# Kernel tuning notes

Measured on AMD Instinct MI355X. Metric: run time of the kernel, lower is better.

## Reference

```python
import jax, jax.numpy as jnp
import numpy as np
from jax import lax

B, T, I, H = 64, 1024, 128, 512
DT = 0.1
EPS = 1e-8
BIG_CLAMP = 50.0
W_SCALE = 0.02  # small init so safe_exp gates stay well-behaved


def _safe_exp(v):
    return jnp.exp(jnp.minimum(v, BIG_CLAMP))


def setup_inputs() -> dict:
    key = jax.random.key(0)
    ks = jax.random.split(key, 9)
    w = lambda k, shape: jax.random.normal(k, shape, jnp.float32) * W_SCALE
    z = lambda: jnp.zeros((H,), jnp.float32)
    return {
        "x": jax.random.normal(ks[0], (B, T, I), jnp.float32),
        "Wsw": w(ks[1], (H, I)), "bsw": z(),
        "Wsm": w(ks[2], (H, I)), "bsm": z(),
        "Wss": w(ks[3], (H, I)), "bss": z(),
        "Wiw": w(ks[4], (H, H)), "biw": z(),
        "Wim": w(ks[5], (H, H)), "bim": z(),
        "Wis": w(ks[6], (H, H)), "bis": z(),
        "Wtcx": w(ks[7], (H, I)),  # time_constant weight, input slice
        "Wtch": w(ks[8], (H, H)),  # time_constant weight, hidden slice
        "btc": z(),
    }


def reference(x, Wsw, bsw, Wsm, bsm, Wss, bss,
              Wiw, biw, Wim, bim, Wis, bis, Wtcx, Wtch, btc):
    # Precompute all x-dependent projections as big GEMMs over (B,T).
    sw = jnp.einsum('bti,hi->bth', x, Wsw) + bsw
    smu = jnp.einsum('bti,hi->bth', x, Wsm) + bsm
    ssig = jnp.einsum('bti,hi->bth', x, Wss) + bss
    sensory = sw * jax.nn.sigmoid(smu) * _safe_exp(ssig)      # (B,T,H)
    tcx = jnp.einsum('bti,hi->bth', x, Wtcx) + btc            # (B,T,H)

    def step(h, inp):
        sens_t, tcx_t = inp                                   # each (B,H)
        tau = jax.nn.softplus(tcx_t + h @ Wtch.T) + 0.1
        inter = (h @ Wiw.T + biw) \
            * jax.nn.sigmoid(h @ Wim.T + bim) \
            * _safe_exp(h @ Wis.T + bis)
        dh_dt = (sens_t + inter - h) / jnp.maximum(tau, EPS)
        h_new = h + DT * dh_dt
        return h_new, h_new

    h0 = jnp.ones((B, H), x.dtype)
    xs = (jnp.swapaxes(sensory, 0, 1), jnp.swapaxes(tcx, 0, 1))  # (T,B,H)
    _, ys = lax.scan(step, h0, xs)
    return jnp.swapaxes(ys, 0, 1)  # (B,T,H)
```

## Files before the change

kernel.cpp:

```cpp
#include <hip/hip_runtime.h>
#include <math.h>

#define NB 64
#define NT 1024
#define NI 128
#define NH 512

typedef unsigned long long u64;

__global__ __launch_bounds__(256) void prep_kernel(
    const float* __restrict__ Wsw, const float* __restrict__ Wsm,
    const float* __restrict__ Wss, const float* __restrict__ Wtcx,
    float* __restrict__ WT_in, u64* __restrict__ htag)
{
  int idx = blockIdx.x * blockDim.x + threadIdx.x;
  int np  = gridDim.x * blockDim.x;
  for (int i = idx; i < NH * NI; i += np) {
    int j = i >> 7, k = i & 127;
    int o = k * 2048 + j * 4;
    WT_in[o + 0] = Wsw[i];
    WT_in[o + 1] = Wsm[i];
    WT_in[o + 2] = Wss[i];
    WT_in[o + 3] = Wtcx[i];
  }
  for (int i = idx; i < 2 * NB * NH; i += np) htag[i] = 0x3F800000ULL;
}

__global__ __launch_bounds__(256, 2) void phase1_kernel(
    const float* __restrict__ x, const float* __restrict__ WT_in,
    const float* __restrict__ bsw, const float* __restrict__ bsm,
    const float* __restrict__ bss, const float* __restrict__ btc,
    float* __restrict__ sens, float* __restrict__ tcx)
{
  __shared__ __align__(16) float xs[32 * NI];
  const int tid = threadIdx.x;
  const int n0  = blockIdx.x * 32;

  const float4* xsrc = (const float4*)(x + (size_t)n0 * NI);
#pragma unroll
  for (int i = 0; i < 4; i++)
    ((float4*)xs)[i * 256 + tid] = xsrc[i * 256 + tid];
  __syncthreads();

  for (int jj = 0; jj < 2; jj++) {
    const int j = tid + jj * 256;
    float4 acc[32];
#pragma unroll
    for (int n = 0; n < 32; n++) acc[n] = make_float4(0.f, 0.f, 0.f, 0.f);

    const float4* wp = (const float4*)WT_in + j;
#pragma unroll 2
    for (int k = 0; k < NI; k++) {
      float4 w = wp[(size_t)k * 512];
#pragma unroll
      for (int n = 0; n < 32; n++) {
        float xv = xs[n * NI + k];
        acc[n].x = fmaf(xv, w.x, acc[n].x);
        acc[n].y = fmaf(xv, w.y, acc[n].y);
        acc[n].z = fmaf(xv, w.z, acc[n].z);
        acc[n].w = fmaf(xv, w.w, acc[n].w);
      }
    }
    const float b0 = bsw[j], b1 = bsm[j], b2v = bss[j], b3 = btc[j];
#pragma unroll 4
    for (int n = 0; n < 32; n++) {
      float sw = acc[n].x + b0;
      float sm = acc[n].y + b1;
      float ss = acc[n].z + b2v;
      float tc = acc[n].w + b3;
      float sig = 1.f / (1.f + expf(-sm));
      float se  = expf(fminf(ss, 50.f));
      size_t o = (size_t)(n0 + n) * NH + j;
      sens[o] = sw * sig * se;
      tcx[o]  = tc;
    }
  }
}

__global__ __launch_bounds__(256, 1) void phase2_kernel(
    const float* __restrict__ Wiw, const float* __restrict__ Wim,
    const float* __restrict__ Wis, const float* __restrict__ Wtch,
    const float* __restrict__ biw, const float* __restrict__ bim,
    const float* __restrict__ bis,
    const float* __restrict__ tcx, float* __restrict__ out,
    u64* __restrict__ htag)
{
  __shared__ __align__(16) float hl[8 * 576];
  __shared__ float red[4 * 528];

  const int tid = threadIdx.x;
  const int wv  = tid >> 6;
  const int ln  = tid & 63;
  const int bg  = blockIdx.x & 7;
  const int js  = blockIdx.x >> 3;

  const int cg = ln & 15;
  const int r  = wv * 4 + (ln >> 4);
  const int k0 = r << 5;

  const int g   = cg & 3;
  const int jl0 = cg >> 2;
  const float* Wp = (g == 0) ? Wiw : (g == 1) ? Wim : (g == 2) ? Wis : Wtch;
  float wreg[4][32];
#pragma unroll
  for (int ci = 0; ci < 4; ci++) {
    const float* wrow = Wp + (size_t)(js * 16 + jl0 + 4 * ci) * NH + k0;
#pragma unroll
    for (int kk = 0; kk < 32; kk++) wreg[ci][kk] = wrow[kk];
  }

  const int ejl = tid & 15;
  const int eb  = tid >> 4;
  const int ej  = js * 16 + ejl;
  float bw = 0.f, bm = 0.f, bs = 0.f;
  if (tid < 128) { bw = biw[ej]; bm = bim[ej]; bs = bis[ej]; }

  u64* const hgrp0 = htag + bg * 4096;
  u64* const hgrp1 = htag + NB * NH + bg * 4096;

  for (int t = 0; t < NT; t++) {
    u64* hsrc = (t & 1) ? hgrp1 : hgrp0;
    u64* hdst = (t & 1) ? hgrp0 : hgrp1;
    const unsigned want = (unsigned)t;

    float sens_v = 0.f, tcx_v = 0.f;
    size_t eidx = 0;
    if (tid < 128) {
      eidx   = ((size_t)(bg * 8 + eb) * NT + t) * NH + ej;
      sens_v = out[eidx];
      tcx_v  = tcx[eidx];
    }

    u64 w[16];
#pragma unroll
    for (int i = 0; i < 16; i++)
      w[i] = __hip_atomic_load(hsrc + i * 256 + tid, __ATOMIC_RELAXED,
                               __HIP_MEMORY_SCOPE_AGENT);
    for (;;) {
      bool ok = true;
#pragma unroll
      for (int i = 0; i < 16; i++) ok = ok && ((unsigned)(w[i] >> 32) == want);
      if (ok) break;
      __builtin_amdgcn_s_sleep(2);
#pragma unroll
      for (int i = 0; i < 16; i++)
        if ((unsigned)(w[i] >> 32) != want)
          w[i] = __hip_atomic_load(hsrc + i * 256 + tid, __ATOMIC_RELAXED,
                                   __HIP_MEMORY_SCOPE_AGENT);
    }

#pragma unroll
    for (int i = 0; i < 16; i++) {
      int f  = i * 256 + tid;
      int b2 = f >> 9, k = f & 511;
      hl[b2 * 576 + (k >> 5) * 36 + (k & 31)] =
          __uint_as_float((unsigned)(w[i] & 0xFFFFFFFFull));
    }
    __syncthreads();

    float acc[4][8];
#pragma unroll
    for (int ci = 0; ci < 4; ci++)
#pragma unroll
      for (int b2 = 0; b2 < 8; b2++) acc[ci][b2] = 0.f;

    const float* hb = hl + r * 36;
#pragma unroll
    for (int b2 = 0; b2 < 8; b2++) {
#pragma unroll
      for (int kc = 0; kc < 32; kc += 4) {
        float4 hv = *(const float4*)(hb + b2 * 576 + kc);
#pragma unroll
        for (int ci = 0; ci < 4; ci++) {
          acc[ci][b2] = fmaf(wreg[ci][kc + 0], hv.x, acc[ci][b2]);
          acc[ci][b2] = fmaf(wreg[ci][kc + 1], hv.y, acc[ci][b2]);
          acc[ci][b2] = fmaf(wreg[ci][kc + 2], hv.z, acc[ci][b2]);
          acc[ci][b2] = fmaf(wreg[ci][kc + 3], hv.w, acc[ci][b2]);
        }
      }
    }

#pragma unroll
    for (int ci = 0; ci < 4; ci++)
#pragma unroll
      for (int b2 = 0; b2 < 8; b2++) {
        float v = acc[ci][b2];
        v += __shfl_xor(v, 16, 64);
        v += __shfl_xor(v, 32, 64);
        acc[ci][b2] = v;
      }
    if (ln < 16) {
#pragma unroll
      for (int ci = 0; ci < 4; ci++)
#pragma unroll
        for (int b2 = 0; b2 < 8; b2++)
          red[wv * 528 + ln * 33 + ci * 8 + b2] = acc[ci][b2];
    }
    float h_old = 0.f;
    if (tid < 128) h_old = hl[eb * 576 + (ej >> 5) * 36 + (ej & 31)];
    __syncthreads();

    if (tid < 128) {
      float vals[4];
#pragma unroll
      for (int g2 = 0; g2 < 4; g2++) {
        int c = ejl * 4 + g2;
        int o = (c & 15) * 33 + (c >> 4) * 8 + eb;
        vals[g2] = red[o] + red[528 + o] + red[1056 + o] + red[1584 + o];
      }
      float iwv = vals[0] + bw;
      float imv = vals[1] + bm;
      float isv = vals[2] + bs;
      float tch = vals[3];
      float z   = tcx_v + tch;
      float tau = fmaxf(z, 0.f) + log1pf(expf(-fabsf(z))) + 0.1f;
      float sig = 1.f / (1.f + expf(-imv));
      float inter = iwv * sig * expf(fminf(isv, 50.f));
      float dh  = (sens_v + inter - h_old) / fmaxf(tau, 1e-8f);
      float hnew = h_old + 0.1f * dh;
      out[eidx] = hnew;
      u64 nw = ((u64)(unsigned)(t + 1) << 32) | (u64)__float_as_uint(hnew);
      __hip_atomic_store(hdst + eb * 512 + ej, nw, __ATOMIC_RELAXED,
                         __HIP_MEMORY_SCOPE_AGENT);
    }
  }
}

extern "C" void kernel_launch(void* const* d_in, const int* in_sizes, int n_in,
                              void* d_out, int out_size, void* d_ws, size_t ws_size,
                              hipStream_t stream) {
  const float* x    = (const float*)d_in[0];
  const float* Wsw  = (const float*)d_in[1];
  const float* bsw  = (const float*)d_in[2];
  const float* Wsm  = (const float*)d_in[3];
  const float* bsm  = (const float*)d_in[4];
  const float* Wss  = (const float*)d_in[5];
  const float* bss  = (const float*)d_in[6];
  const float* Wiw  = (const float*)d_in[7];
  const float* biw  = (const float*)d_in[8];
  const float* Wim  = (const float*)d_in[9];
  const float* bim  = (const float*)d_in[10];
  const float* Wis  = (const float*)d_in[11];
  const float* bis  = (const float*)d_in[12];
  const float* Wtcx = (const float*)d_in[13];
  const float* Wtch = (const float*)d_in[14];
  const float* btc  = (const float*)d_in[15];
  float* out = (float*)d_out;

  float* ws     = (float*)d_ws;
  float* WT_in  = ws;
  float* tcx    = ws + 262144;
  u64*   htag   = (u64*)(tcx + (size_t)NB * NT * NH);

  hipLaunchKernelGGL(prep_kernel, dim3(256), dim3(256), 0, stream,
                     Wsw, Wsm, Wss, Wtcx, WT_in, htag);

  hipLaunchKernelGGL(phase1_kernel, dim3(NB * NT / 32), dim3(256), 0, stream,
                     x, WT_in, bsw, bsm, bss, btc, out, tcx);

  hipLaunchKernelGGL(phase2_kernel, dim3(256), dim3(256), 0, stream,
                     Wiw, Wim, Wis, Wtch, biw, bim, bis,
                     tcx, out, htag);
}
```

Before: 8.124 ms.

## Replace tagged hidden-state polling with plain floats and a per-group arrival counter

Each recurrent step used to pack the step tag into the upper half of every 64-bit hidden-state word, and every thread spun on all 16 of its tagged words. Now the hidden state is stored as plain 32-bit floats. Each block drains its stores, then bumps one atomic counter per batch group, and readers spin only on that counter before bulk-loading the data. This halves the bytes exchanged per step and cuts polling traffic to a single address. In exchange it adds a block-wide barrier, a memory wait and an extra atomic round trip on the critical path of every step.

```diff
diff --git a/kernel.cpp b/kernel.cpp
--- a/kernel.cpp
+++ b/kernel.cpp
@@ -11,7 +11,8 @@
 __global__ __launch_bounds__(256) void prep_kernel(
     const float* __restrict__ Wsw, const float* __restrict__ Wsm,
     const float* __restrict__ Wss, const float* __restrict__ Wtcx,
-    float* __restrict__ WT_in, u64* __restrict__ htag)
+    float* __restrict__ WT_in, float* __restrict__ hdat,
+    unsigned* __restrict__ cnt)
 {
   int idx = blockIdx.x * blockDim.x + threadIdx.x;
   int np  = gridDim.x * blockDim.x;
@@ -23,7 +24,8 @@
     WT_in[o + 2] = Wss[i];
     WT_in[o + 3] = Wtcx[i];
   }
-  for (int i = idx; i < 2 * NB * NH; i += np) htag[i] = 0x3F800000ULL;
+  for (int i = idx; i < 2 * NB * NH; i += np) hdat[i] = 1.0f;
+  for (int i = idx; i < 256; i += np) cnt[i] = 0u;
 }
 
 __global__ __launch_bounds__(256, 2) void phase1_kernel(
@@ -83,7 +85,7 @@
     const float* __restrict__ biw, const float* __restrict__ bim,
     const float* __restrict__ bis,
     const float* __restrict__ tcx, float* __restrict__ out,
-    u64* __restrict__ htag)
+    float* __restrict__ hdat, unsigned* __restrict__ cnt)
 {
   __shared__ __align__(16) float hl[8 * 576];
   __shared__ float red[4 * 528];
@@ -115,13 +117,14 @@
   float bw = 0.f, bm = 0.f, bs = 0.f;
   if (tid < 128) { bw = biw[ej]; bm = bim[ej]; bs = bis[ej]; }
 
-  u64* const hgrp0 = htag + bg * 4096;
-  u64* const hgrp1 = htag + NB * NH + bg * 4096;
+  float* const hp0 = hdat + bg * 4096;
+  float* const hp1 = hdat + NB * NH + bg * 4096;
+  unsigned* const cbg = cnt + bg * 32;
 
   for (int t = 0; t < NT; t++) {
-    u64* hsrc = (t & 1) ? hgrp1 : hgrp0;
-    u64* hdst = (t & 1) ? hgrp0 : hgrp1;
-    const unsigned want = (unsigned)t;
+    const u64* dsrc = (const u64*)((t & 1) ? hp1 : hp0);
+    unsigned*  ddst = (unsigned*)((t & 1) ? hp0 : hp1);
+    const unsigned want = 32u * (unsigned)t;
 
     float sens_v = 0.f, tcx_v = 0.f;
     size_t eidx = 0;
@@ -131,30 +134,28 @@
       tcx_v  = tcx[eidx];
     }
 
-    u64 w[16];
-#pragma unroll
-    for (int i = 0; i < 16; i++)
-      w[i] = __hip_atomic_load(hsrc + i * 256 + tid, __ATOMIC_RELAXED,
+    if (t > 0) {
+      unsigned c;
+      do {
+        c = __hip_atomic_load(cbg, __ATOMIC_RELAXED, __HIP_MEMORY_SCOPE_AGENT);
+      } while (c < want);
+      asm volatile("" ::: "memory");
+    }
+
+    u64 w[8];
+#pragma unroll
+    for (int i = 0; i < 8; i++)
+      w[i] = __hip_atomic_load(dsrc + i * 256 + tid, __ATOMIC_RELAXED,
                                __HIP_MEMORY_SCOPE_AGENT);
-    for (;;) {
-      bool ok = true;
-#pragma unroll
-      for (int i = 0; i < 16; i++) ok = ok && ((unsigned)(w[i] >> 32) == want);
-      if (ok) break;
-      __builtin_amdgcn_s_sleep(2);
-#pragma unroll
-      for (int i = 0; i < 16; i++)
-        if ((unsigned)(w[i] >> 32) != want)
-          w[i] = __hip_atomic_load(hsrc + i * 256 + tid, __ATOMIC_RELAXED,
-                                   __HIP_MEMORY_SCOPE_AGENT);
-    }
-
-#pragma unroll
-    for (int i = 0; i < 16; i++) {
+
+#pragma unroll
+    for (int i = 0; i < 8; i++) {
       int f  = i * 256 + tid;
-      int b2 = f >> 9, k = f & 511;
-      hl[b2 * 576 + (k >> 5) * 36 + (k & 31)] =
-          __uint_as_float((unsigned)(w[i] & 0xFFFFFFFFull));
+      int b2 = f >> 8;
+      int k  = (f & 255) << 1;
+      float lo = __uint_as_float((unsigned)(w[i] & 0xFFFFFFFFull));
+      float hi = __uint_as_float((unsigned)(w[i] >> 32));
+      *(float2*)&hl[b2 * 576 + (k >> 5) * 36 + (k & 31)] = make_float2(lo, hi);
     }
     __syncthreads();
 
@@ -218,11 +219,15 @@
       float inter = iwv * sig * expf(fminf(isv, 50.f));
       float dh  = (sens_v + inter - h_old) / fmaxf(tau, 1e-8f);
       float hnew = h_old + 0.1f * dh;
+      __hip_atomic_store(ddst + eb * 512 + ej, __float_as_uint(hnew),
+                         __ATOMIC_RELAXED, __HIP_MEMORY_SCOPE_AGENT);
       out[eidx] = hnew;
-      u64 nw = ((u64)(unsigned)(t + 1) << 32) | (u64)__float_as_uint(hnew);
-      __hip_atomic_store(hdst + eb * 512 + ej, nw, __ATOMIC_RELAXED,
-                         __HIP_MEMORY_SCOPE_AGENT);
-    }
+      asm volatile("s_waitcnt vmcnt(0)" ::: "memory");
+    }
+    __syncthreads();
+    if (tid == 0)
+      __hip_atomic_fetch_add(cbg, 1u, __ATOMIC_RELAXED,
+                             __HIP_MEMORY_SCOPE_AGENT);
   }
 }
 
@@ -250,15 +255,16 @@
   float* ws     = (float*)d_ws;
   float* WT_in  = ws;
   float* tcx    = ws + 262144;
-  u64*   htag   = (u64*)(tcx + (size_t)NB * NT * NH);
+  float* hdat   = tcx + (size_t)NB * NT * NH;
+  unsigned* cnt = (unsigned*)(hdat + 2 * NB * NH);
 
   hipLaunchKernelGGL(prep_kernel, dim3(256), dim3(256), 0, stream,
-                     Wsw, Wsm, Wss, Wtcx, WT_in, htag);
+                     Wsw, Wsm, Wss, Wtcx, WT_in, hdat, cnt);
 
   hipLaunchKernelGGL(phase1_kernel, dim3(NB * NT / 32), dim3(256), 0, stream,
                      x, WT_in, bsw, bsm, bss, btc, out, tcx);
 
   hipLaunchKernelGGL(phase2_kernel, dim3(256), dim3(256), 0, stream,
                      Wiw, Wim, Wis, Wtch, biw, bim, bis,
-                     tcx, out, htag);
-}
+                     tcx, out, hdat, cnt);
+}
```

Result: faster. 7.535 ms (-7.2%).

## Interleave two batch groups per block to hide recurrent h-exchange latency

Applied to the files above, without the earlier changes.

The persistent recurrent kernel now runs 128 blocks, each owning two batch groups (bgA and bgB) with separate shared h buffers. While one group's step is being computed, the atomic loads that poll the other group's h tags are already in flight. Each block also issues the next step's loads for group A before finishing group B. The aim is to overlap the cross-block synchronisation latency with computation, at the cost of halving the block count so each block does twice the work per step. The poll sleep is shortened, and the output store now follows the tag publish.

```diff
diff --git a/kernel.cpp b/kernel.cpp
--- a/kernel.cpp
+++ b/kernel.cpp
@@ -77,6 +77,101 @@
   }
 }
 
+#define ISSUE16(W, SRC)                                                     \
+  _Pragma("unroll")                                                         \
+  for (int i = 0; i < 16; i++)                                              \
+    W[i] = __hip_atomic_load((SRC) + i * 256 + tid, __ATOMIC_RELAXED,       \
+                             __HIP_MEMORY_SCOPE_AGENT);
+
+#define CHECK16(W, SRC, WANT)                                               \
+  for (;;) {                                                                \
+    bool ok = true;                                                         \
+    _Pragma("unroll")                                                       \
+    for (int i = 0; i < 16; i++)                                            \
+      ok = ok && ((unsigned)(W[i] >> 32) == (WANT));                        \
+    if (ok) break;                                                          \
+    __builtin_amdgcn_s_sleep(1);                                            \
+    _Pragma("unroll")                                                       \
+    for (int i = 0; i < 16; i++)                                            \
+      if ((unsigned)(W[i] >> 32) != (WANT))                                 \
+        W[i] = __hip_atomic_load((SRC) + i * 256 + tid, __ATOMIC_RELAXED,   \
+                                 __HIP_MEMORY_SCOPE_AGENT);                 \
+  }
+
+#define DO_PHASE(HL, W, DST, EIDX, SENSV, TCXV, TP1)                        \
+  {                                                                         \
+    _Pragma("unroll")                                                       \
+    for (int i = 0; i < 16; i++) {                                          \
+      int f = i * 256 + tid;                                                \
+      int b2 = f >> 9, k = f & 511;                                         \
+      HL[b2 * 576 + (k >> 5) * 36 + (k & 31)] =                             \
+          __uint_as_float((unsigned)(W[i] & 0xFFFFFFFFull));                \
+    }                                                                       \
+    __syncthreads();                                                        \
+    float acc[4][8];                                                        \
+    _Pragma("unroll")                                                       \
+    for (int ci = 0; ci < 4; ci++)                                          \
+      _Pragma("unroll")                                                     \
+      for (int b2 = 0; b2 < 8; b2++) acc[ci][b2] = 0.f;                     \
+    const float* hb = HL + r * 36;                                          \
+    _Pragma("unroll")                                                       \
+    for (int b2 = 0; b2 < 8; b2++) {                                        \
+      _Pragma("unroll")                                                     \
+      for (int kc = 0; kc < 32; kc += 4) {                                  \
+        float4 hv = *(const float4*)(hb + b2 * 576 + kc);                   \
+        _Pragma("unroll")                                                   \
+        for (int ci = 0; ci < 4; ci++) {                                    \
+          acc[ci][b2] = fmaf(wreg[ci][kc + 0], hv.x, acc[ci][b2]);          \
+          acc[ci][b2] = fmaf(wreg[ci][kc + 1], hv.y, acc[ci][b2]);          \
+          acc[ci][b2] = fmaf(wreg[ci][kc + 2], hv.z, acc[ci][b2]);          \
+          acc[ci][b2] = fmaf(wreg[ci][kc + 3], hv.w, acc[ci][b2]);          \
+        }                                                                   \
+      }                                                                     \
+    }                                                                       \
+    _Pragma("unroll")                                                       \
+    for (int ci = 0; ci < 4; ci++)                                          \
+      _Pragma("unroll")                                                     \
+      for (int b2 = 0; b2 < 8; b2++) {                                      \
+        float v = acc[ci][b2];                                              \
+        v += __shfl_xor(v, 16, 64);                                         \
+        v += __shfl_xor(v, 32, 64);                                         \
+        acc[ci][b2] = v;                                                    \
+      }                                                                     \
+    if (ln < 16) {                                                          \
+      _Pragma("unroll")                                                     \
+      for (int ci = 0; ci < 4; ci++)                                        \
+        _Pragma("unroll")                                                   \
+        for (int b2 = 0; b2 < 8; b2++)                                      \
+          red[wv * 528 + ln * 33 + ci * 8 + b2] = acc[ci][b2];              \
+    }                                                                       \
+    float h_old = 0.f;                                                      \
+    if (tid < 128) h_old = HL[eb * 576 + (ej >> 5) * 36 + (ej & 31)];       \
+    __syncthreads();                                                        \
+    if (tid < 128) {                                                        \
+      float vals[4];                                                        \
+      _Pragma("unroll")                                                     \
+      for (int g2 = 0; g2 < 4; g2++) {                                      \
+        int c = ejl * 4 + g2;                                               \
+        int o = (c & 15) * 33 + (c >> 4) * 8 + eb;                          \
+        vals[g2] = red[o] + red[528 + o] + red[1056 + o] + red[1584 + o];   \
+      }                                                                     \
+      float iwv = vals[0] + bw;                                             \
+      float imv = vals[1] + bm;                                             \
+      float isv = vals[2] + bs;                                             \
+      float tch = vals[3];                                                  \
+      float z   = (TCXV) + tch;                                             \
+      float tau = fmaxf(z, 0.f) + log1pf(expf(-fabsf(z))) + 0.1f;           \
+      float sig = 1.f / (1.f + expf(-imv));                                 \
+      float inter = iwv * sig * expf(fminf(isv, 50.f));                     \
+      float dh  = ((SENSV) + inter - h_old) / fmaxf(tau, 1e-8f);            \
+      float hnew = h_old + 0.1f * dh;                                       \
+      u64 nw = ((u64)(unsigned)(TP1) << 32) | (u64)__float_as_uint(hnew);   \
+      __hip_atomic_store((DST) + eb * 512 + ej, nw, __ATOMIC_RELAXED,       \
+                         __HIP_MEMORY_SCOPE_AGENT);                         \
+      out[EIDX] = hnew;                                                     \
+    }                                                                       \
+  }
+
 __global__ __launch_bounds__(256, 1) void phase2_kernel(
     const float* __restrict__ Wiw, const float* __restrict__ Wim,
     const float* __restrict__ Wis, const float* __restrict__ Wtch,
@@ -85,14 +180,17 @@
     const float* __restrict__ tcx, float* __restrict__ out,
     u64* __restrict__ htag)
 {
-  __shared__ __align__(16) float hl[8 * 576];
+  __shared__ __align__(16) float hlA[8 * 576];
+  __shared__ __align__(16) float hlB[8 * 576];
   __shared__ float red[4 * 528];
 
   const int tid = threadIdx.x;
   const int wv  = tid >> 6;
   const int ln  = tid & 63;
-  const int bg  = blockIdx.x & 7;
-  const int js  = blockIdx.x >> 3;
+  const int pc  = blockIdx.x & 3;
+  const int js  = blockIdx.x >> 2;
+  const int bgA = pc;
+  const int bgB = pc + 4;
 
   const int cg = ln & 15;
   const int r  = wv * 4 + (ln >> 4);
@@ -115,114 +213,41 @@
   float bw = 0.f, bm = 0.f, bs = 0.f;
   if (tid < 128) { bw = biw[ej]; bm = bim[ej]; bs = bis[ej]; }
 
-  u64* const hgrp0 = htag + bg * 4096;
-  u64* const hgrp1 = htag + NB * NH + bg * 4096;
+  u64* const hA0 = htag + bgA * 4096;
+  u64* const hA1 = htag + NB * NH + bgA * 4096;
+  u64* const hB0 = htag + bgB * 4096;
+  u64* const hB1 = htag + NB * NH + bgB * 4096;
+
+  u64 wA[16], wB[16];
+  ISSUE16(wA, hA0);
 
   for (int t = 0; t < NT; t++) {
-    u64* hsrc = (t & 1) ? hgrp1 : hgrp0;
-    u64* hdst = (t & 1) ? hgrp0 : hgrp1;
+    u64* sA = (t & 1) ? hA1 : hA0;
+    u64* dA = (t & 1) ? hA0 : hA1;
+    u64* sB = (t & 1) ? hB1 : hB0;
+    u64* dB = (t & 1) ? hB0 : hB1;
     const unsigned want = (unsigned)t;
 
-    float sens_v = 0.f, tcx_v = 0.f;
-    size_t eidx = 0;
+    float sensA = 0.f, tcxA = 0.f, sensB = 0.f, tcxB = 0.f;
+    size_t eiA = 0, eiB = 0;
     if (tid < 128) {
-      eidx   = ((size_t)(bg * 8 + eb) * NT + t) * NH + ej;
-      sens_v = out[eidx];
-      tcx_v  = tcx[eidx];
+      eiA   = ((size_t)(bgA * 8 + eb) * NT + t) * NH + ej;
+      eiB   = ((size_t)(bgB * 8 + eb) * NT + t) * NH + ej;
+      sensA = out[eiA];
+      tcxA  = tcx[eiA];
+      sensB = out[eiB];
+      tcxB  = tcx[eiB];
     }
 
-    u64 w[16];
-#pragma unroll
-    for (int i = 0; i < 16; i++)
-      w[i] = __hip_atomic_load(hsrc + i * 256 + tid, __ATOMIC_RELAXED,
-                               __HIP_MEMORY_SCOPE_AGENT);
-    for (;;) {
-      bool ok = true;
-#pragma unroll
-      for (int i = 0; i < 16; i++) ok = ok && ((unsigned)(w[i] >> 32) == want);
-      if (ok) break;
-      __builtin_amdgcn_s_sleep(2);
-#pragma unroll
-      for (int i = 0; i < 16; i++)
-        if ((unsigned)(w[i] >> 32) != want)
-          w[i] = __hip_atomic_load(hsrc + i * 256 + tid, __ATOMIC_RELAXED,
-                                   __HIP_MEMORY_SCOPE_AGENT);
-    }
-
-#pragma unroll
-    for (int i = 0; i < 16; i++) {
-      int f  = i * 256 + tid;
-      int b2 = f >> 9, k = f & 511;
-      hl[b2 * 576 + (k >> 5) * 36 + (k & 31)] =
-          __uint_as_float((unsigned)(w[i] & 0xFFFFFFFFull));
-    }
-    __syncthreads();
-
-    float acc[4][8];
-#pragma unroll
-    for (int ci = 0; ci < 4; ci++)
-#pragma unroll
-      for (int b2 = 0; b2 < 8; b2++) acc[ci][b2] = 0.f;
-
-    const float* hb = hl + r * 36;
-#pragma unroll
-    for (int b2 = 0; b2 < 8; b2++) {
-#pragma unroll
-      for (int kc = 0; kc < 32; kc += 4) {
-        float4 hv = *(const float4*)(hb + b2 * 576 + kc);
-#pragma unroll
-        for (int ci = 0; ci < 4; ci++) {
-          acc[ci][b2] = fmaf(wreg[ci][kc + 0], hv.x, acc[ci][b2]);
-          acc[ci][b2] = fmaf(wreg[ci][kc + 1], hv.y, acc[ci][b2]);
-          acc[ci][b2] = fmaf(wreg[ci][kc + 2], hv.z, acc[ci][b2]);
-          acc[ci][b2] = fmaf(wreg[ci][kc + 3], hv.w, acc[ci][b2]);
-        }
-      }
-    }
-
-#pragma unroll
-    for (int ci = 0; ci < 4; ci++)
-#pragma unroll
-      for (int b2 = 0; b2 < 8; b2++) {
-        float v = acc[ci][b2];
-        v += __shfl_xor(v, 16, 64);
-        v += __shfl_xor(v, 32, 64);
-        acc[ci][b2] = v;
-      }
-    if (ln < 16) {
-#pragma unroll
-      for (int ci = 0; ci < 4; ci++)
-#pragma unroll
-        for (int b2 = 0; b2 < 8; b2++)
-          red[wv * 528 + ln * 33 + ci * 8 + b2] = acc[ci][b2];
-    }
-    float h_old = 0.f;
-    if (tid < 128) h_old = hl[eb * 576 + (ej >> 5) * 36 + (ej & 31)];
-    __syncthreads();
-
-    if (tid < 128) {
-      float vals[4];
-#pragma unroll
-      for (int g2 = 0; g2 < 4; g2++) {
-        int c = ejl * 4 + g2;
-        int o = (c & 15) * 33 + (c >> 4) * 8 + eb;
-        vals[g2] = red[o] + red[528 + o] + red[1056 + o] + red[1584 + o];
-      }
-      float iwv = vals[0] + bw;
-      float imv = vals[1] + bm;
-      float isv = vals[2] + bs;
-      float tch = vals[3];
-      float z   = tcx_v + tch;
-      float tau = fmaxf(z, 0.f) + log1pf(expf(-fabsf(z))) + 0.1f;
-      float sig = 1.f / (1.f + expf(-imv));
-      float inter = iwv * sig * expf(fminf(isv, 50.f));
-      float dh  = (sens_v + inter - h_old) / fmaxf(tau, 1e-8f);
-      float hnew = h_old + 0.1f * dh;
-      out[eidx] = hnew;
-      u64 nw = ((u64)(unsigned)(t + 1) << 32) | (u64)__float_as_uint(hnew);
-      __hip_atomic_store(hdst + eb * 512 + ej, nw, __ATOMIC_RELAXED,
-                         __HIP_MEMORY_SCOPE_AGENT);
-    }
+    CHECK16(wA, sA, want);
+    ISSUE16(wB, sB);
+
+    DO_PHASE(hlA, wA, dA, eiA, sensA, tcxA, t + 1);
+
+    CHECK16(wB, sB, want);
+    if (t + 1 < NT) ISSUE16(wA, dA);
+
+    DO_PHASE(hlB, wB, dB, eiB, sensB, tcxB, t + 1);
   }
 }
 
@@ -258,7 +283,7 @@
   hipLaunchKernelGGL(phase1_kernel, dim3(NB * NT / 32), dim3(256), 0, stream,
                      x, WT_in, bsw, bsm, bss, btc, out, tcx);
 
-  hipLaunchKernelGGL(phase2_kernel, dim3(256), dim3(256), 0, stream,
+  hipLaunchKernelGGL(phase2_kernel, dim3(128), dim3(256), 0, stream,
                      Wiw, Wim, Wis, Wtch, biw, bim, bis,
                      tcx, out, htag);
 }
```

After: 22.07 ms. 172% more time.
